# Kernel optimization log

Hardware: AMD Instinct MI355X
Metric: run time of the kernel (lower is better)

Reference implementation:

```python
import jax, jax.numpy as jnp
import numpy as np

B, N, DEG = 64, 512, 16        # graphs, nodes per graph, avg degree
C, HID = 10, 128               # input feat dim (== num_classes quirk), hidden
E = B * N * DEG                # total edges (fixed; pooling masks edges)


def _gcn(x, W, b, src, dst, emask, n):
    # PyG GCNConv: add self-loops, symmetric norm D^-1/2 (A+I) D^-1/2 (XW) + b
    h = x @ W
    deg = jax.ops.segment_sum(emask, dst, num_segments=n) + 1.0  # +1 self-loop
    dinv = jax.lax.rsqrt(deg)
    norm = dinv[src] * dinv[dst] * emask
    agg = jax.ops.segment_sum(h[src] * norm[:, None], dst, num_segments=n)
    return agg + h * (dinv * dinv)[:, None] + b  # self-loop term + bias


def _sag_pool(x, src, dst, emask, Wp, bp, n_per):
    # SAGPooling: score = tanh(GCN(x)); per-graph top-k (ratio=0.5); x' = x[perm]*score
    n = x.shape[0]
    score = jnp.tanh(_gcn(x, Wp, bp, src, dst, emask, n)[:, 0])
    k = n_per // 2
    vals, idx = jax.lax.top_k(score.reshape(B, n_per), k)  # [B,k]
    perm = (idx + (jnp.arange(B) * n_per)[:, None]).reshape(-1)
    xk = x[perm] * vals.reshape(-1)[:, None]
    # relabel edges; drop edges touching removed nodes via mask (fixed E)
    mapping = jnp.full((n,), -1, jnp.int32).at[perm].set(
        jnp.arange(B * k, dtype=jnp.int32))
    ns, nd = mapping[src], mapping[dst]
    nmask = emask * ((ns >= 0) & (nd >= 0)).astype(emask.dtype)
    return xk, jnp.maximum(ns, 0), jnp.maximum(nd, 0), nmask, k


def _readout(x, k):
    # global max pool || global mean pool (all kept nodes are real, no padding)
    xg = x.reshape(B, k, -1)
    return jnp.concatenate([xg.max(axis=1), xg.mean(axis=1)], axis=1)


def setup_inputs() -> dict:
    key = jax.random.key(0)
    ks = jax.random.split(key, 16)
    x = jax.random.normal(ks[0], (B * N, C), jnp.float32)
    off = jnp.repeat(jnp.arange(B, dtype=jnp.int32) * N, N * DEG)
    src = jax.random.randint(ks[1], (E,), 0, N, jnp.int32) + off
    dst = jax.random.randint(ks[2], (E,), 0, N, jnp.int32) + off
    p = lambda k, s: jax.random.normal(k, s, jnp.float32) * 0.05
    return {
        "x": x, "src": src, "dst": dst,
        "W1": p(ks[3], (C, HID)), "b1": jnp.zeros((HID,), jnp.float32),
        "W2": p(ks[4], (HID, HID)), "b2": jnp.zeros((HID,), jnp.float32),
        "W3": p(ks[5], (HID, HID)), "b3": jnp.zeros((HID,), jnp.float32),
        "Wp": p(ks[6], (HID, 1)), "bp": jnp.zeros((1,), jnp.float32),
        "L1W": p(ks[7], (2 * HID, HID)), "L1b": jnp.zeros((HID,), jnp.float32),
        "L2W": p(ks[8], (HID, HID // 2)), "L2b": jnp.zeros((HID // 2,), jnp.float32),
    }


def reference(x, src, dst, W1, b1, W2, b2, W3, b3, Wp, bp, L1W, L1b, L2W, L2b):
    emask = jnp.ones((E,), jnp.float32)
    h = jax.nn.relu(_gcn(x, W1, b1, src, dst, emask, B * N))
    h, src, dst, emask, k = _sag_pool(h, src, dst, emask, Wp, bp, N)
    x1 = _readout(h, k)
    h = jax.nn.relu(_gcn(h, W2, b2, src, dst, emask, B * k))
    h, src, dst, emask, k = _sag_pool(h, src, dst, emask, Wp, bp, k)
    x2 = _readout(h, k)
    h = jax.nn.relu(_gcn(h, W3, b3, src, dst, emask, B * k))
    h, src, dst, emask, k = _sag_pool(h, src, dst, emask, Wp, bp, k)
    x3 = _readout(h, k)
    z = x1 + x2 + x3
    z = jax.nn.relu(z @ L1W + L1b)
    # dropout inactive in eval mode
    z = jax.nn.relu(z @ L2W + L2b)
    return jax.nn.log_softmax(z, axis=1)
```

## Files before the change

kernel.cpp:

```cpp
#include <hip/hip_runtime.h>
#include <math.h>

#define BGR 64
#define N0 512
#define E_TOT (BGR*N0*16)
#define EPG 8192
#define EIT 16
#define HID 128
#define LOFF2 32768
#define LOFF3 49152

#define HSW(r,l) (((r)<<3) | (((l)+(r))&7))

__device__ __forceinline__ void bitonic_sort(float* sv, int* si, float v, int idx,
                                             int t, int nper, bool act){
  for (int kk = 2; kk <= nper; kk <<= 1){
    for (int jj = kk >> 1; jj > 0; jj >>= 1){
      if (jj >= 64){
        if (act){ sv[t] = v; si[t] = idx; }
        __syncthreads();
        if (act){
          int p = t ^ jj;
          float pv = sv[p]; int pi = si[p];
          bool amLower = (t & jj) == 0;
          bool dirDesc = (t & kk) == 0;
          bool betterMine = (v > pv) || (v == pv && idx < pi);
          if ((amLower == dirDesc) != betterMine){ v = pv; idx = pi; }
        }
        __syncthreads();
      } else if (act){
        float pv = __shfl_xor(v, jj);
        int   pi = __shfl_xor(idx, jj);
        bool amLower = (t & jj) == 0;
        bool dirDesc = (t & kk) == 0;
        bool betterMine = (v > pv) || (v == pv && idx < pi);
        if ((amLower == dirDesc) != betterMine){ v = pv; idx = pi; }
      }
    }
  }
  if (act){ sv[t] = v; si[t] = idx; }
  __syncthreads();
}

__device__ __forceinline__ void relabel_pre(
    int2* __restrict__ edges, int2* __restrict__ csr, const int* si,
    int* map_, int* sb, int* cur, float* dl, int* wsum,
    int* __restrict__ rowptr, int* __restrict__ cnt, float* __restrict__ dinv,
    const int2* epre,
    int t, int nper, int k, int gbase, int gbnew, int ebase, int loff){
  if (t < nper) map_[t] = -1;
  if (t < k) sb[t] = 0;
  __syncthreads();
  if (t < k) map_[si[t]] = t;
  __syncthreads();
  int2 ebuf[8];
  #pragma unroll
  for (int it = 0; it < 8; it++){
    int2 e = epre[it];
    int2 ne = make_int2(-1, 0);
    if (e.x >= 0){
      int ns = map_[e.x - gbase], nd = map_[e.y - gbase];
      if (ns >= 0 && nd >= 0){
        ne = make_int2(gbnew + ns, gbnew + nd);
        atomicAdd(&sb[nd], 1);
      }
    }
    ebuf[it] = ne;
    edges[ebase + it*1024 + t] = ne;
  }
  __syncthreads();
  int vdeg = (t < k) ? sb[t] : 0;
  int lane = t & 63, wid = t >> 6;
  int x = vdeg;
  #pragma unroll
  for (int off = 1; off < 64; off <<= 1){
    int y = __shfl_up(x, off);
    if (lane >= off) x += y;
  }
  if (t < k && lane == 63) wsum[wid] = x;
  __syncthreads();
  if (t < k){
    int prefix = 0;
    #pragma unroll
    for (int wj = 0; wj < 4; wj++) prefix += (wj < wid) ? wsum[wj] : 0;
    int excl = x + prefix - vdeg;
    rowptr[loff + gbnew + t] = ebase + excl;
    cnt[loff + gbnew + t] = vdeg;
    cur[t] = excl;
    float dv = rsqrtf((float)vdeg + 1.f);
    dl[t] = dv;
    dinv[loff + gbnew + t] = dv;
  }
  __syncthreads();
  #pragma unroll
  for (int it = 0; it < 8; it++){
    int2 e = ebuf[it];
    if (e.x >= 0){
      int sl = e.x - gbnew, dc = e.y - gbnew;
      int pos = atomicAdd(&cur[dc], 1);
      csr[ebase + pos] = make_int2(e.x, __float_as_int(dl[sl]*dl[dc]));
    }
  }
  __syncthreads();
}

__global__ __launch_bounds__(512) void k_topo0(
    const int* __restrict__ s0, const int* __restrict__ d0,
    int2* __restrict__ edges, int* __restrict__ cnt, int* __restrict__ rowptr,
    float* __restrict__ dinv, int2* __restrict__ csr){
  __shared__ int   deg[512];
  __shared__ int   cur[512];
  __shared__ float dl[512];
  __shared__ int   wsum[8];
  int g = (blockIdx.x & 7)*8 + (blockIdx.x >> 3);
  int t = threadIdx.x;
  int gbase = g*N0, ebase = g*EPG;
  deg[t] = 0;
  __syncthreads();
  int2 ebuf[EIT];
  #pragma unroll
  for (int it = 0; it < EIT; it++){
    int i = ebase + it*512 + t;
    int2 e = make_int2(s0[i], d0[i]);
    ebuf[it] = e;
    edges[i] = e;
    atomicAdd(&deg[e.y - gbase], 1);
  }
  __syncthreads();
  int vdeg = deg[t];
  int lane = t & 63, wid = t >> 6;
  int x = vdeg;
  #pragma unroll
  for (int off = 1; off < 64; off <<= 1){
    int y = __shfl_up(x, off);
    if (lane >= off) x += y;
  }
  if (lane == 63) wsum[wid] = x;
  __syncthreads();
  int prefix = 0;
  #pragma unroll
  for (int wj = 0; wj < 8; wj++) prefix += (wj < wid) ? wsum[wj] : 0;
  int excl = x + prefix - vdeg;
  rowptr[gbase + t] = ebase + excl;
  cnt[gbase + t] = vdeg;
  cur[t] = excl;
  float dv = rsqrtf((float)vdeg + 1.f);
  dl[t] = dv;
  dinv[gbase + t] = dv;
  __syncthreads();
  #pragma unroll
  for (int it = 0; it < EIT; it++){
    int2 e = ebuf[it];
    int sl = e.x - gbase, dc = e.y - gbase;
    int pos = atomicAdd(&cur[dc], 1);
    csr[ebase + pos] = make_int2(e.x, __float_as_int(dl[sl]*dl[dc]));
  }
}

__global__ __launch_bounds__(512) void k_l1_fused(
    const float* __restrict__ x, const float* __restrict__ W1,
    const int2* __restrict__ csr, const int* __restrict__ rowptr,
    const int* __restrict__ cnt, const float* __restrict__ dinv,
    const float* __restrict__ b1, const float* __restrict__ Wp,
    float4* __restrict__ gout4, float* __restrict__ hp_part){
  extern __shared__ float hl[];
  int b = blockIdx.x;
  int xcd = b & 7, idx = b >> 3;
  int graph = xcd*8 + (idx >> 3);
  int sub = idx & 7;
  int qf = sub >> 1, half = sub & 1;
  int t = threadIdx.x;
  int gbase = graph*N0;
  int fp = t & 31;
  int f = qf*32 + fp;
  float wcol[10];
  #pragma unroll
  for (int k = 0; k < 10; k++) wcol[k] = W1[k*HID + f];
  for (int n = t >> 5; n < N0; n += 16){
    const float* xr = x + (gbase + n)*10;
    float acc = 0.f;
    #pragma unroll
    for (int k = 0; k < 10; k++) acc += xr[k]*wcol[k];
    hl[n*32 + ((((fp>>2)+n)&7)<<2) + (fp&3)] = acc;
  }
  __syncthreads();
  const float4* hl4 = (const float4*)hl;
  int l = t & 7, grp = t >> 3;
  float4 bb = ((const float4*)b1)[qf*8 + l];
  float4 wp = ((const float4*)Wp)[qf*8 + l];
  int n0 = half*256;
  for (int nl = n0 + grp; nl < n0 + 256; nl += 64){
    int node = gbase + nl;
    int start = rowptr[node], c = cnt[node];
    float4 acc = make_float4(0.f,0.f,0.f,0.f);
    int j = 0;
    for (; j + 4 <= c; j += 4){
      int2 e0 = csr[start+j],   e1 = csr[start+j+1];
      int2 e2 = csr[start+j+2], e3 = csr[start+j+3];
      float4 h0 = hl4[HSW(e0.x - gbase, l)];
      float4 h1 = hl4[HSW(e1.x - gbase, l)];
      float4 h2 = hl4[HSW(e2.x - gbase, l)];
      float4 h3 = hl4[HSW(e3.x - gbase, l)];
      float w0 = __int_as_float(e0.y), w1 = __int_as_float(e1.y);
      float w2 = __int_as_float(e2.y), w3 = __int_as_float(e3.y);
      acc.x += w0*h0.x + w1*h1.x + w2*h2.x + w3*h3.x;
      acc.y += w0*h0.y + w1*h1.y + w2*h2.y + w3*h3.y;
      acc.z += w0*h0.z + w1*h1.z + w2*h2.z + w3*h3.z;
      acc.w += w0*h0.w + w1*h1.w + w2*h2.w + w3*h3.w;
    }
    for (; j < c; j++){
      int2 e = csr[start + j];
      float wgt = __int_as_float(e.y);
      float4 hv = hl4[HSW(e.x - gbase, l)];
      acc.x += wgt*hv.x; acc.y += wgt*hv.y; acc.z += wgt*hv.z; acc.w += wgt*hv.w;
    }
    float di = dinv[node], dd = di*di;
    float4 hs = hl4[HSW(nl, l)];
    float4 v;
    v.x = fmaxf(acc.x + hs.x*dd + bb.x, 0.f);
    v.y = fmaxf(acc.y + hs.y*dd + bb.y, 0.f);
    v.z = fmaxf(acc.z + hs.z*dd + bb.z, 0.f);
    v.w = fmaxf(acc.w + hs.w*dd + bb.w, 0.f);
    gout4[node*32 + qf*8 + l] = v;
    float contrib = v.x*wp.x + v.y*wp.y + v.z*wp.z + v.w*wp.w;
    #pragma unroll
    for (int off = 4; off; off >>= 1) contrib += __shfl_down(contrib, off, 8);
    if (l == 0) hp_part[qf*32768 + node] = contrib;
  }
}

__global__ __launch_bounds__(1024) void k_mega1(
    const float4* __restrict__ gout4, const float* __restrict__ hppt,
    int2* __restrict__ csr, int* __restrict__ rowptr, int* __restrict__ cnt,
    float* __restrict__ dinv, const float* __restrict__ bp,
    int2* __restrict__ edges, int* __restrict__ sig, float* __restrict__ svg,
    float* __restrict__ z){
  __shared__ float sv[512];
  __shared__ int   si[512];
  __shared__ float hpl[512];
  __shared__ union UA {
    float spart[1024];
    struct { float4 pmx[16][32]; float4 psm[16][32]; } ro;
    struct { int map_[512]; int sb[512]; int cur[256]; } rl;
  } u;
  __shared__ float dl[256];
  __shared__ int   wsum[4];
  int g = (blockIdx.x & 7)*8 + (blockIdx.x >> 3);
  int t = threadIdx.x;
  int gbase = g*N0, ebase = g*EPG, gb2 = g*256;
  float bp0 = bp[0];
  int2 epre[8];
  #pragma unroll
  for (int it = 0; it < 8; it++) epre[it] = edges[ebase + it*1024 + t];
  if (t < 512){
    int node = gbase + t;
    hpl[t] = hppt[node] + hppt[32768+node] + hppt[65536+node] + hppt[98304+node];
  }
  __syncthreads();
  {
    int n = t & 511, p = t >> 9;
    int start = rowptr[gbase + n], c = cnt[gbase + n];
    int lo = (c*p) >> 1, hi = (c*(p+1)) >> 1;
    float a = 0.f;
    for (int j = lo; j < hi; j++){
      int2 e = csr[start + j];
      a += __int_as_float(e.y)*hpl[e.x - gbase];
    }
    u.spart[t] = a;
  }
  __syncthreads();
  float v = 0.f; int idx = t;
  if (t < 512){
    float a = u.spart[t] + u.spart[t + 512];
    float di = dinv[gbase + t];
    v = tanhf(a + hpl[t]*di*di + bp0);
  }
  __syncthreads();
  bitonic_sort(sv, si, v, idx, t, 512, t < 512);
  if (t < 256){ sig[g*512 + t] = si[t]; svg[g*512 + t] = sv[t]; }
  int l = t & 31, j0 = t >> 5;
  if (t < 512){
    float4 mx = make_float4(-INFINITY,-INFINITY,-INFINITY,-INFINITY);
    float4 sm = make_float4(0.f,0.f,0.f,0.f);
    for (int j = j0; j < 256; j += 16){
      float val = sv[j]; int row = si[j];
      float4 hv = gout4[(gbase + row)*32 + l];
      float4 o = make_float4(hv.x*val, hv.y*val, hv.z*val, hv.w*val);
      mx.x = fmaxf(mx.x, o.x); mx.y = fmaxf(mx.y, o.y);
      mx.z = fmaxf(mx.z, o.z); mx.w = fmaxf(mx.w, o.w);
      sm.x += o.x; sm.y += o.y; sm.z += o.z; sm.w += o.w;
    }
    u.ro.pmx[j0][l] = mx; u.ro.psm[j0][l] = sm;
  }
  __syncthreads();
  if (t < 32){
    float4 M = u.ro.pmx[0][t], S = u.ro.psm[0][t];
    #pragma unroll
    for (int q = 1; q < 16; q++){
      float4 m2 = u.ro.pmx[q][t], s2 = u.ro.psm[q][t];
      M.x = fmaxf(M.x, m2.x); M.y = fmaxf(M.y, m2.y);
      M.z = fmaxf(M.z, m2.z); M.w = fmaxf(M.w, m2.w);
      S.x += s2.x; S.y += s2.y; S.z += s2.z; S.w += s2.w;
    }
    float ki = 1.f/256.f;
    float* zp = z + g*256;
    zp[t*4+0] = M.x; zp[t*4+1] = M.y; zp[t*4+2] = M.z; zp[t*4+3] = M.w;
    zp[128+t*4+0] = S.x*ki; zp[128+t*4+1] = S.y*ki;
    zp[128+t*4+2] = S.z*ki; zp[128+t*4+3] = S.w*ki;
  }
  __syncthreads();
  relabel_pre(edges, csr, si, u.rl.map_, u.rl.sb, u.rl.cur, dl, wsum,
              rowptr, cnt, dinv, epre, t, 512, 256, gbase, gb2, ebase, LOFF2);
}

__global__ __launch_bounds__(512) void k_lvl2(
    const float4* __restrict__ gout4,
    const int* __restrict__ sig, const float* __restrict__ svg,
    const float* __restrict__ W2, const float* __restrict__ b2,
    const float* __restrict__ Wp,
    const int2* __restrict__ csr, const int* __restrict__ rowptr,
    const int* __restrict__ cnt, const float* __restrict__ dinv,
    float4* __restrict__ g2out4, float* __restrict__ hp2){
  __shared__ float hL[256*HID];
  int b = blockIdx.x;
  int jb = b & 63, sub = b >> 6;
  int g = (jb & 7)*8 + (jb >> 3);
  int t = threadIdx.x;
  int gbase = g*N0, gb2 = g*256;
  {
    int foct = t & 15, rg = t >> 4;
    int f0 = foct*8, rbase = rg*8;
    int ri[8]; float rv[8];
    #pragma unroll
    for (int q = 0; q < 8; q++){
      ri[q] = sig[g*512 + rbase + q];
      rv[q] = svg[g*512 + rbase + q];
    }
    float4 accA[8], accB[8];
    #pragma unroll
    for (int q = 0; q < 8; q++){
      accA[q] = make_float4(0.f,0.f,0.f,0.f);
      accB[q] = make_float4(0.f,0.f,0.f,0.f);
    }
    for (int i = 0; i < HID; i += 4){
      float4 wa[4], wb[4];
      #pragma unroll
      for (int ii = 0; ii < 4; ii++){
        wa[ii] = *(const float4*)(W2 + (i+ii)*HID + f0);
        wb[ii] = *(const float4*)(W2 + (i+ii)*HID + f0 + 4);
      }
      #pragma unroll
      for (int q = 0; q < 8; q++){
        float4 xv = gout4[(gbase + ri[q])*32 + (i>>2)];
        float vx = xv.x*rv[q], vy = xv.y*rv[q], vz = xv.z*rv[q], vw = xv.w*rv[q];
        accA[q].x += vx*wa[0].x + vy*wa[1].x + vz*wa[2].x + vw*wa[3].x;
        accA[q].y += vx*wa[0].y + vy*wa[1].y + vz*wa[2].y + vw*wa[3].y;
        accA[q].z += vx*wa[0].z + vy*wa[1].z + vz*wa[2].z + vw*wa[3].z;
        accA[q].w += vx*wa[0].w + vy*wa[1].w + vz*wa[2].w + vw*wa[3].w;
        accB[q].x += vx*wb[0].x + vy*wb[1].x + vz*wb[2].x + vw*wb[3].x;
        accB[q].y += vx*wb[0].y + vy*wb[1].y + vz*wb[2].y + vw*wb[3].y;
        accB[q].z += vx*wb[0].z + vy*wb[1].z + vz*wb[2].z + vw*wb[3].z;
        accB[q].w += vx*wb[0].w + vy*wb[1].w + vz*wb[2].w + vw*wb[3].w;
      }
    }
    #pragma unroll
    for (int q = 0; q < 8; q++){
      *(float4*)(hL + (rbase+q)*HID + f0) = accA[q];
      *(float4*)(hL + (rbase+q)*HID + f0 + 4) = accB[q];
    }
  }
  __syncthreads();
  const float4* hL4 = (const float4*)hL;
  int l = t & 31, grpn = t >> 5;
  float4 bb = ((const float4*)b2)[l];
  float4 wp = ((const float4*)Wp)[l];
  for (int it = 0; it < 4; it++){
    int n = sub*64 + it*16 + grpn;
    int node = gb2 + n;
    int start = rowptr[LOFF2 + node], c = cnt[LOFF2 + node];
    float4 acc = make_float4(0.f,0.f,0.f,0.f);
    int j = 0;
    for (; j + 4 <= c; j += 4){
      int2 e0 = csr[start+j],   e1 = csr[start+j+1];
      int2 e2 = csr[start+j+2], e3 = csr[start+j+3];
      float4 h0 = hL4[(e0.x - gb2)*32 + l];
      float4 h1 = hL4[(e1.x - gb2)*32 + l];
      float4 h2 = hL4[(e2.x - gb2)*32 + l];
      float4 h3 = hL4[(e3.x - gb2)*32 + l];
      float w0 = __int_as_float(e0.y), w1 = __int_as_float(e1.y);
      float w2 = __int_as_float(e2.y), w3 = __int_as_float(e3.y);
      acc.x += w0*h0.x + w1*h1.x + w2*h2.x + w3*h3.x;
      acc.y += w0*h0.y + w1*h1.y + w2*h2.y + w3*h3.y;
      acc.z += w0*h0.z + w1*h1.z + w2*h2.z + w3*h3.z;
      acc.w += w0*h0.w + w1*h1.w + w2*h2.w + w3*h3.w;
    }
    for (; j < c; j++){
      int2 e = csr[start + j];
      float wgt = __int_as_float(e.y);
      float4 hv = hL4[(e.x - gb2)*32 + l];
      acc.x += wgt*hv.x; acc.y += wgt*hv.y; acc.z += wgt*hv.z; acc.w += wgt*hv.w;
    }
    float di = dinv[LOFF2 + node], dd = di*di;
    float4 hs = hL4[n*32 + l];
    float4 v;
    v.x = fmaxf(acc.x + hs.x*dd + bb.x, 0.f);
    v.y = fmaxf(acc.y + hs.y*dd + bb.y, 0.f);
    v.z = fmaxf(acc.z + hs.z*dd + bb.z, 0.f);
    v.w = fmaxf(acc.w + hs.w*dd + bb.w, 0.f);
    g2out4[node*32 + l] = v;
    float contrib = v.x*wp.x + v.y*wp.y + v.z*wp.z + v.w*wp.w;
    #pragma unroll
    for (int off = 16; off; off >>= 1) contrib += __shfl_down(contrib, off, 32);
    if (l == 0) hp2[node] = contrib;
  }
}

__global__ __launch_bounds__(1024) void k_mega2(
    const float4* __restrict__ g2out4, const float* __restrict__ hp2,
    int2* __restrict__ csr, int* __restrict__ rowptr, int* __restrict__ cnt,
    float* __restrict__ dinv, const float* __restrict__ bp,
    int2* __restrict__ edges, int* __restrict__ sig, float* __restrict__ svg,
    float* __restrict__ z){
  __shared__ float sv[256];
  __shared__ int   si[256];
  __shared__ float hpl[256];
  __shared__ union UB {
    float spart[1024];
    struct { float4 pmx[16][32]; float4 psm[16][32]; } ro;
    struct { int map_[256]; int sb[128]; int cur[128]; } rl;
  } u;
  __shared__ float dl[128];
  __shared__ int   wsum[4];
  int g = (blockIdx.x & 7)*8 + (blockIdx.x >> 3);
  int t = threadIdx.x;
  int gb2 = g*256, gb3 = g*128, ebase = g*EPG;
  float bp0 = bp[0];
  int2 epre[8];
  #pragma unroll
  for (int it = 0; it < 8; it++) epre[it] = edges[ebase + it*1024 + t];
  if (t < 256) hpl[t] = hp2[gb2 + t];
  __syncthreads();
  {
    int n = t & 255, p = t >> 8;
    int start = rowptr[LOFF2 + gb2 + n], c = cnt[LOFF2 + gb2 + n];
    int lo = (c*p) >> 2, hi = (c*(p+1)) >> 2;
    float a = 0.f;
    for (int j = lo; j < hi; j++){
      int2 e = csr[start + j];
      a += __int_as_float(e.y)*hpl[e.x - gb2];
    }
    u.spart[t] = a;
  }
  __syncthreads();
  float v = 0.f; int idx = t;
  if (t < 256){
    float a = u.spart[t] + u.spart[t+256] + u.spart[t+512] + u.spart[t+768];
    float di = dinv[LOFF2 + gb2 + t];
    v = tanhf(a + hpl[t]*di*di + bp0);
  }
  __syncthreads();
  bitonic_sort(sv, si, v, idx, t, 256, t < 256);
  if (t < 128){ sig[g*512 + t] = si[t]; svg[g*512 + t] = sv[t]; }
  int l = t & 31, j0 = t >> 5;
  if (t < 512){
    float4 mx = make_float4(-INFINITY,-INFINITY,-INFINITY,-INFINITY);
    float4 sm = make_float4(0.f,0.f,0.f,0.f);
    for (int j = j0; j < 128; j += 16){
      float val = sv[j]; int row = si[j];
      float4 hv = g2out4[(gb2 + row)*32 + l];
      float4 o = make_float4(hv.x*val, hv.y*val, hv.z*val, hv.w*val);
      mx.x = fmaxf(mx.x, o.x); mx.y = fmaxf(mx.y, o.y);
      mx.z = fmaxf(mx.z, o.z); mx.w = fmaxf(mx.w, o.w);
      sm.x += o.x; sm.y += o.y; sm.z += o.z; sm.w += o.w;
    }
    u.ro.pmx[j0][l] = mx; u.ro.psm[j0][l] = sm;
  }
  __syncthreads();
  if (t < 32){
    float4 M = u.ro.pmx[0][t], S = u.ro.psm[0][t];
    #pragma unroll
    for (int q = 1; q < 16; q++){
      float4 m2 = u.ro.pmx[q][t], s2 = u.ro.psm[q][t];
      M.x = fmaxf(M.x, m2.x); M.y = fmaxf(M.y, m2.y);
      M.z = fmaxf(M.z, m2.z); M.w = fmaxf(M.w, m2.w);
      S.x += s2.x; S.y += s2.y; S.z += s2.z; S.w += s2.w;
    }
    float ki = 1.f/128.f;
    float* zp = z + g*256;
    zp[t*4+0] += M.x; zp[t*4+1] += M.y; zp[t*4+2] += M.z; zp[t*4+3] += M.w;
    zp[128+t*4+0] += S.x*ki; zp[128+t*4+1] += S.y*ki;
    zp[128+t*4+2] += S.z*ki; zp[128+t*4+3] += S.w*ki;
  }
  __syncthreads();
  relabel_pre(edges, csr, si, u.rl.map_, u.rl.sb, u.rl.cur, dl, wsum,
              rowptr, cnt, dinv, epre, t, 256, 128, gb2, gb3, ebase, LOFF3);
}

__global__ __launch_bounds__(512) void k_lvl3(
    const float4* __restrict__ g2out4,
    const int* __restrict__ sig, const float* __restrict__ svg,
    const float* __restrict__ W3, const float* __restrict__ b3,
    const float* __restrict__ Wp,
    const int2* __restrict__ csr, const int* __restrict__ rowptr,
    const int* __restrict__ cnt, const float* __restrict__ dinv,
    float4* __restrict__ g3out4, float* __restrict__ hp3){
  __shared__ float hL[128*HID];
  int b = blockIdx.x;
  int jb = b & 63, sub = b >> 6;
  int g = (jb & 7)*8 + (jb >> 3);
  int t = threadIdx.x;
  int gb2 = g*256, gb3 = g*128;
  {
    int foct = t & 15, rg = t >> 4;
    int f0 = foct*8, rbase = rg*4;
    int ri[4]; float rv[4];
    #pragma unroll
    for (int q = 0; q < 4; q++){
      ri[q] = sig[g*512 + rbase + q];
      rv[q] = svg[g*512 + rbase + q];
    }
    float4 accA[4], accB[4];
    #pragma unroll
    for (int q = 0; q < 4; q++){
      accA[q] = make_float4(0.f,0.f,0.f,0.f);
      accB[q] = make_float4(0.f,0.f,0.f,0.f);
    }
    for (int i = 0; i < HID; i += 4){
      float4 wa[4], wb[4];
      #pragma unroll
      for (int ii = 0; ii < 4; ii++){
        wa[ii] = *(const float4*)(W3 + (i+ii)*HID + f0);
        wb[ii] = *(const float4*)(W3 + (i+ii)*HID + f0 + 4);
      }
      #pragma unroll
      for (int q = 0; q < 4; q++){
        float4 xv = g2out4[(gb2 + ri[q])*32 + (i>>2)];
        float vx = xv.x*rv[q], vy = xv.y*rv[q], vz = xv.z*rv[q], vw = xv.w*rv[q];
        accA[q].x += vx*wa[0].x + vy*wa[1].x + vz*wa[2].x + vw*wa[3].x;
        accA[q].y += vx*wa[0].y + vy*wa[1].y + vz*wa[2].y + vw*wa[3].y;
        accA[q].z += vx*wa[0].z + vy*wa[1].z + vz*wa[2].z + vw*wa[3].z;
        accA[q].w += vx*wa[0].w + vy*wa[1].w + vz*wa[2].w + vw*wa[3].w;
        accB[q].x += vx*wb[0].x + vy*wb[1].x + vz*wb[2].x + vw*wb[3].x;
        accB[q].y += vx*wb[0].y + vy*wb[1].y + vz*wb[2].y + vw*wb[3].y;
        accB[q].z += vx*wb[0].z + vy*wb[1].z + vz*wb[2].z + vw*wb[3].z;
        accB[q].w += vx*wb[0].w + vy*wb[1].w + vz*wb[2].w + vw*wb[3].w;
      }
    }
    #pragma unroll
    for (int q = 0; q < 4; q++){
      *(float4*)(hL + (rbase+q)*HID + f0) = accA[q];
      *(float4*)(hL + (rbase+q)*HID + f0 + 4) = accB[q];
    }
  }
  __syncthreads();
  const float4* hL4 = (const float4*)hL;
  int l = t & 31, grpn = t >> 5;
  float4 bb = ((const float4*)b3)[l];
  float4 wp = ((const float4*)Wp)[l];
  for (int it = 0; it < 2; it++){
    int n = sub*32 + it*16 + grpn;
    int node = gb3 + n;
    int start = rowptr[LOFF3 + node], c = cnt[LOFF3 + node];
    float4 acc = make_float4(0.f,0.f,0.f,0.f);
    int j = 0;
    for (; j + 4 <= c; j += 4){
      int2 e0 = csr[start+j],   e1 = csr[start+j+1];
      int2 e2 = csr[start+j+2], e3 = csr[start+j+3];
      float4 h0 = hL4[(e0.x - gb3)*32 + l];
      float4 h1 = hL4[(e1.x - gb3)*32 + l];
      float4 h2 = hL4[(e2.x - gb3)*32 + l];
      float4 h3 = hL4[(e3.x - gb3)*32 + l];
      float w0 = __int_as_float(e0.y), w1 = __int_as_float(e1.y);
      float w2 = __int_as_float(e2.y), w3 = __int_as_float(e3.y);
      acc.x += w0*h0.x + w1*h1.x + w2*h2.x + w3*h3.x;
      acc.y += w0*h0.y + w1*h1.y + w2*h2.y + w3*h3.y;
      acc.z += w0*h0.z + w1*h1.z + w2*h2.z + w3*h3.z;
      acc.w += w0*h0.w + w1*h1.w + w2*h2.w + w3*h3.w;
    }
    for (; j < c; j++){
      int2 e = csr[start + j];
      float wgt = __int_as_float(e.y);
      float4 hv = hL4[(e.x - gb3)*32 + l];
      acc.x += wgt*hv.x; acc.y += wgt*hv.y; acc.z += wgt*hv.z; acc.w += wgt*hv.w;
    }
    float di = dinv[LOFF3 + node], dd = di*di;
    float4 hs = hL4[n*32 + l];
    float4 v;
    v.x = fmaxf(acc.x + hs.x*dd + bb.x, 0.f);
    v.y = fmaxf(acc.y + hs.y*dd + bb.y, 0.f);
    v.z = fmaxf(acc.z + hs.z*dd + bb.z, 0.f);
    v.w = fmaxf(acc.w + hs.w*dd + bb.w, 0.f);
    g3out4[node*32 + l] = v;
    float contrib = v.x*wp.x + v.y*wp.y + v.z*wp.z + v.w*wp.w;
    #pragma unroll
    for (int off = 16; off; off >>= 1) contrib += __shfl_down(contrib, off, 32);
    if (l == 0) hp3[node] = contrib;
  }
}

__global__ __launch_bounds__(1024) void k_mega3(
    const float4* __restrict__ g3out4, const float* __restrict__ hp3,
    const int2* __restrict__ csr, const int* __restrict__ rowptr,
    const int* __restrict__ cnt, const float* __restrict__ dinv,
    const float* __restrict__ bp, float* __restrict__ z,
    const float* __restrict__ L1W, const float* __restrict__ L1b,
    const float* __restrict__ L2W, const float* __restrict__ L2b,
    float* __restrict__ out){
  __shared__ float sv[128];
  __shared__ int   si[128];
  __shared__ float hpl[128];
  __shared__ union UC {
    float spart[1024];
    struct { float4 pmx[16][32]; float4 psm[16][32]; } ro;
  } u;
  __shared__ float zr[256];
  __shared__ float h1l[128];
  __shared__ float h2l[64];
  __shared__ float red[2];
  int g = (blockIdx.x & 7)*8 + (blockIdx.x >> 3);
  int t = threadIdx.x;
  int gb3 = g*128;
  float bp0 = bp[0];
  if (t < 128) hpl[t] = hp3[gb3 + t];
  __syncthreads();
  {
    int n = t & 127, p = t >> 7;
    int start = rowptr[LOFF3 + gb3 + n], c = cnt[LOFF3 + gb3 + n];
    int lo = (c*p) >> 3, hi = (c*(p+1)) >> 3;
    float a = 0.f;
    for (int j = lo; j < hi; j++){
      int2 e = csr[start + j];
      a += __int_as_float(e.y)*hpl[e.x - gb3];
    }
    u.spart[t] = a;
  }
  __syncthreads();
  float v = 0.f; int idx = t;
  if (t < 128){
    float a = 0.f;
    #pragma unroll
    for (int pp = 0; pp < 8; pp++) a += u.spart[t + pp*128];
    float di = dinv[LOFF3 + gb3 + t];
    v = tanhf(a + hpl[t]*di*di + bp0);
  }
  __syncthreads();
  bitonic_sort(sv, si, v, idx, t, 128, t < 128);
  int l = t & 31, j0 = t >> 5;
  if (t < 512){
    float4 mx = make_float4(-INFINITY,-INFINITY,-INFINITY,-INFINITY);
    float4 sm = make_float4(0.f,0.f,0.f,0.f);
    for (int j = j0; j < 64; j += 16){
      float val = sv[j]; int row = si[j];
      float4 hv = g3out4[(gb3 + row)*32 + l];
      float4 o = make_float4(hv.x*val, hv.y*val, hv.z*val, hv.w*val);
      mx.x = fmaxf(mx.x, o.x); mx.y = fmaxf(mx.y, o.y);
      mx.z = fmaxf(mx.z, o.z); mx.w = fmaxf(mx.w, o.w);
      sm.x += o.x; sm.y += o.y; sm.z += o.z; sm.w += o.w;
    }
    u.ro.pmx[j0][l] = mx; u.ro.psm[j0][l] = sm;
  }
  __syncthreads();
  if (t < 32){
    float4 M = u.ro.pmx[0][t], S = u.ro.psm[0][t];
    #pragma unroll
    for (int q = 1; q < 16; q++){
      float4 m2 = u.ro.pmx[q][t], s2 = u.ro.psm[q][t];
      M.x = fmaxf(M.x, m2.x); M.y = fmaxf(M.y, m2.y);
      M.z = fmaxf(M.z, m2.z); M.w = fmaxf(M.w, m2.w);
      S.x += s2.x; S.y += s2.y; S.z += s2.z; S.w += s2.w;
    }
    float ki = 1.f/64.f;
    float* zp = z + g*256;
    zr[t*4+0] = zp[t*4+0] + M.x; zr[t*4+1] = zp[t*4+1] + M.y;
    zr[t*4+2] = zp[t*4+2] + M.z; zr[t*4+3] = zp[t*4+3] + M.w;
    zr[128+t*4+0] = zp[128+t*4+0] + S.x*ki;
    zr[128+t*4+1] = zp[128+t*4+1] + S.y*ki;
    zr[128+t*4+2] = zp[128+t*4+2] + S.z*ki;
    zr[128+t*4+3] = zp[128+t*4+3] + S.w*ki;
  }
  __syncthreads();
  if (t < 128){
    float a = L1b[t];
    for (int i = 0; i < 256; i++) a += zr[i]*L1W[i*128 + t];
    h1l[t] = fmaxf(a, 0.f);
  }
  __syncthreads();
  if (t < 64){
    float a = L2b[t];
    for (int i = 0; i < 128; i++) a += h1l[i]*L2W[i*64 + t];
    h2l[t] = fmaxf(a, 0.f);
  }
  __syncthreads();
  if (t == 0){
    float mxv = -INFINITY;
    for (int i = 0; i < 64; i++) mxv = fmaxf(mxv, h2l[i]);
    float s = 0.f;
    for (int i = 0; i < 64; i++) s += expf(h2l[i] - mxv);
    red[0] = mxv; red[1] = logf(s);
  }
  __syncthreads();
  if (t < 64) out[g*64 + t] = h2l[t] - red[0] - red[1];
}

extern "C" void kernel_launch(void* const* d_in, const int* in_sizes, int n_in,
                              void* d_out, int out_size, void* d_ws, size_t ws_size,
                              hipStream_t stream){
  (void)in_sizes; (void)n_in; (void)out_size; (void)ws_size;
  const float* x0  = (const float*)d_in[0];
  const int*   s0  = (const int*)  d_in[1];
  const int*   d0  = (const int*)  d_in[2];
  const float* W1  = (const float*)d_in[3];  const float* b1 = (const float*)d_in[4];
  const float* W2  = (const float*)d_in[5];  const float* b2 = (const float*)d_in[6];
  const float* W3  = (const float*)d_in[7];  const float* b3 = (const float*)d_in[8];
  const float* Wp  = (const float*)d_in[9];  const float* bp = (const float*)d_in[10];
  const float* L1W = (const float*)d_in[11]; const float* L1b = (const float*)d_in[12];
  const float* L2W = (const float*)d_in[13]; const float* L2b = (const float*)d_in[14];
  float* out = (float*)d_out;

  float* w = (float*)d_ws;
  float* gout1 = w; w += 32768*HID;
  float* gout2 = w; w += 16384*HID;
  float* gout3 = w; w += 8192*HID;
  float* dinvv = w; w += 65536;
  float* hppt  = w; w += 4*32768;
  float* hp2   = w; w += 16384;
  float* hp3   = w; w += 8192;
  float* z     = w; w += BGR*256;
  float* svg   = w; w += 32768;
  int* sig     = (int*)w; w += 32768;
  int* cnt     = (int*)w; w += 65536;
  int* rowptr  = (int*)w; w += 65536;
  int2* edges  = (int2*)w; w += 2*E_TOT;
  int2* csr    = (int2*)w; w += 2*E_TOT;

  k_topo0<<<BGR, 512, 0, stream>>>(s0, d0, edges, cnt, rowptr, dinvv, csr);
  k_l1_fused<<<512, 512, 65536, stream>>>(x0, W1, csr, rowptr, cnt, dinvv,
                                          b1, Wp, (float4*)gout1, hppt);
  k_mega1<<<BGR, 1024, 0, stream>>>((const float4*)gout1, hppt, csr, rowptr,
                                    cnt, dinvv, bp, edges, sig, svg, z);
  k_lvl2<<<4*BGR, 512, 0, stream>>>((const float4*)gout1, sig, svg, W2, b2, Wp,
                                    csr, rowptr, cnt, dinvv,
                                    (float4*)gout2, hp2);
  k_mega2<<<BGR, 1024, 0, stream>>>((const float4*)gout2, hp2, csr, rowptr,
                                    cnt, dinvv, bp, edges, sig, svg, z);
  k_lvl3<<<4*BGR, 512, 0, stream>>>((const float4*)gout2, sig, svg, W3, b3, Wp,
                                    csr, rowptr, cnt, dinvv,
                                    (float4*)gout3, hp3);
  k_mega3<<<BGR, 1024, 0, stream>>>((const float4*)gout3, hp3, csr, rowptr,
                                    cnt, dinvv, bp, z,
                                    L1W, L1b, L2W, L2b, out);
}
```

Before: 257.8 us.

## Split level-2/3 GCN blocks by feature slice instead of node slice

```diff
diff --git a/kernel.cpp b/kernel.cpp
--- a/kernel.cpp
+++ b/kernel.cpp
@@ -320,62 +320,51 @@
     const float* __restrict__ Wp,
     const int2* __restrict__ csr, const int* __restrict__ rowptr,
     const int* __restrict__ cnt, const float* __restrict__ dinv,
-    float4* __restrict__ g2out4, float* __restrict__ hp2){
-  __shared__ float hL[256*HID];
+    float4* __restrict__ g2out4, float* __restrict__ hp2p){
+  __shared__ float hL[256*32];
   int b = blockIdx.x;
-  int jb = b & 63, sub = b >> 6;
+  int jb = b & 63, s = b >> 6;
   int g = (jb & 7)*8 + (jb >> 3);
   int t = threadIdx.x;
   int gbase = g*N0, gb2 = g*256;
+  float4* hL4 = (float4*)hL;
   {
-    int foct = t & 15, rg = t >> 4;
-    int f0 = foct*8, rbase = rg*8;
-    int ri[8]; float rv[8];
-    #pragma unroll
-    for (int q = 0; q < 8; q++){
+    int f4 = t & 7, rg = t >> 3;
+    int rbase = rg*4;
+    const float* Wb = W2 + s*32 + f4*4;
+    int ri[4]; float rv[4];
+    #pragma unroll
+    for (int q = 0; q < 4; q++){
       ri[q] = sig[g*512 + rbase + q];
       rv[q] = svg[g*512 + rbase + q];
     }
-    float4 accA[8], accB[8];
-    #pragma unroll
-    for (int q = 0; q < 8; q++){
-      accA[q] = make_float4(0.f,0.f,0.f,0.f);
-      accB[q] = make_float4(0.f,0.f,0.f,0.f);
-    }
+    float4 acc[4];
+    #pragma unroll
+    for (int q = 0; q < 4; q++) acc[q] = make_float4(0.f,0.f,0.f,0.f);
     for (int i = 0; i < HID; i += 4){
-      float4 wa[4], wb[4];
+      float4 w0 = *(const float4*)(Wb + (i+0)*HID);
+      float4 w1 = *(const float4*)(Wb + (i+1)*HID);
+      float4 w2 = *(const float4*)(Wb + (i+2)*HID);
+      float4 w3 = *(const float4*)(Wb + (i+3)*HID);
       #pragma unroll
-      for (int ii = 0; ii < 4; ii++){
-        wa[ii] = *(const float4*)(W2 + (i+ii)*HID + f0);
-        wb[ii] = *(const float4*)(W2 + (i+ii)*HID + f0 + 4);
-      }
-      #pragma unroll
-      for (int q = 0; q < 8; q++){
+      for (int q = 0; q < 4; q++){
         float4 xv = gout4[(gbase + ri[q])*32 + (i>>2)];
         float vx = xv.x*rv[q], vy = xv.y*rv[q], vz = xv.z*rv[q], vw = xv.w*rv[q];
-        accA[q].x += vx*wa[0].x + vy*wa[1].x + vz*wa[2].x + vw*wa[3].x;
-        accA[q].y += vx*wa[0].y + vy*wa[1].y + vz*wa[2].y + vw*wa[3].y;
-        accA[q].z += vx*wa[0].z + vy*wa[1].z + vz*wa[2].z + vw*wa[3].z;
-        accA[q].w += vx*wa[0].w + vy*wa[1].w + vz*wa[2].w + vw*wa[3].w;
-        accB[q].x += vx*wb[0].x + vy*wb[1].x + vz*wb[2].x + vw*wb[3].x;
-        accB[q].y += vx*wb[0].y + vy*wb[1].y + vz*wb[2].y + vw*wb[3].y;
-        accB[q].z += vx*wb[0].z + vy*wb[1].z + vz*wb[2].z + vw*wb[3].z;
-        accB[q].w += vx*wb[0].w + vy*wb[1].w + vz*wb[2].w + vw*wb[3].w;
+        acc[q].x += vx*w0.x + vy*w1.x + vz*w2.x + vw*w3.x;
+        acc[q].y += vx*w0.y + vy*w1.y + vz*w2.y + vw*w3.y;
+        acc[q].z += vx*w0.z + vy*w1.z + vz*w2.z + vw*w3.z;
+        acc[q].w += vx*w0.w + vy*w1.w + vz*w2.w + vw*w3.w;
       }
     }
     #pragma unroll
-    for (int q = 0; q < 8; q++){
-      *(float4*)(hL + (rbase+q)*HID + f0) = accA[q];
-      *(float4*)(hL + (rbase+q)*HID + f0 + 4) = accB[q];
-    }
-  }
-  __syncthreads();
-  const float4* hL4 = (const float4*)hL;
-  int l = t & 31, grpn = t >> 5;
-  float4 bb = ((const float4*)b2)[l];
-  float4 wp = ((const float4*)Wp)[l];
+    for (int q = 0; q < 4; q++) hL4[HSW(rbase+q, f4)] = acc[q];
+  }
+  __syncthreads();
+  int l = t & 7, grpn = t >> 3;
+  float4 bb = ((const float4*)b2)[s*8 + l];
+  float4 wp = ((const float4*)Wp)[s*8 + l];
   for (int it = 0; it < 4; it++){
-    int n = sub*64 + it*16 + grpn;
+    int n = it*64 + grpn;
     int node = gb2 + n;
     int start = rowptr[LOFF2 + node], c = cnt[LOFF2 + node];
     float4 acc = make_float4(0.f,0.f,0.f,0.f);
@@ -383,10 +372,10 @@
     for (; j + 4 <= c; j += 4){
       int2 e0 = csr[start+j],   e1 = csr[start+j+1];
       int2 e2 = csr[start+j+2], e3 = csr[start+j+3];
-      float4 h0 = hL4[(e0.x - gb2)*32 + l];
-      float4 h1 = hL4[(e1.x - gb2)*32 + l];
-      float4 h2 = hL4[(e2.x - gb2)*32 + l];
-      float4 h3 = hL4[(e3.x - gb2)*32 + l];
+      float4 h0 = hL4[HSW(e0.x - gb2, l)];
+      float4 h1 = hL4[HSW(e1.x - gb2, l)];
+      float4 h2 = hL4[HSW(e2.x - gb2, l)];
+      float4 h3 = hL4[HSW(e3.x - gb2, l)];
       float w0 = __int_as_float(e0.y), w1 = __int_as_float(e1.y);
       float w2 = __int_as_float(e2.y), w3 = __int_as_float(e3.y);
       acc.x += w0*h0.x + w1*h1.x + w2*h2.x + w3*h3.x;
@@ -397,26 +386,26 @@
     for (; j < c; j++){
       int2 e = csr[start + j];
       float wgt = __int_as_float(e.y);
-      float4 hv = hL4[(e.x - gb2)*32 + l];
+      float4 hv = hL4[HSW(e.x - gb2, l)];
       acc.x += wgt*hv.x; acc.y += wgt*hv.y; acc.z += wgt*hv.z; acc.w += wgt*hv.w;
     }
     float di = dinv[LOFF2 + node], dd = di*di;
-    float4 hs = hL4[n*32 + l];
+    float4 hs = hL4[HSW(n, l)];
     float4 v;
     v.x = fmaxf(acc.x + hs.x*dd + bb.x, 0.f);
     v.y = fmaxf(acc.y + hs.y*dd + bb.y, 0.f);
     v.z = fmaxf(acc.z + hs.z*dd + bb.z, 0.f);
     v.w = fmaxf(acc.w + hs.w*dd + bb.w, 0.f);
-    g2out4[node*32 + l] = v;
+    g2out4[node*32 + s*8 + l] = v;
     float contrib = v.x*wp.x + v.y*wp.y + v.z*wp.z + v.w*wp.w;
     #pragma unroll
-    for (int off = 16; off; off >>= 1) contrib += __shfl_down(contrib, off, 32);
-    if (l == 0) hp2[node] = contrib;
+    for (int off = 4; off; off >>= 1) contrib += __shfl_down(contrib, off, 8);
+    if (l == 0) hp2p[s*16384 + node] = contrib;
   }
 }
 
 __global__ __launch_bounds__(1024) void k_mega2(
-    const float4* __restrict__ g2out4, const float* __restrict__ hp2,
+    const float4* __restrict__ g2out4, const float* __restrict__ hp2p,
     int2* __restrict__ csr, int* __restrict__ rowptr, int* __restrict__ cnt,
     float* __restrict__ dinv, const float* __restrict__ bp,
     int2* __restrict__ edges, int* __restrict__ sig, float* __restrict__ svg,
@@ -438,7 +427,10 @@
   int2 epre[8];
   #pragma unroll
   for (int it = 0; it < 8; it++) epre[it] = edges[ebase + it*1024 + t];
-  if (t < 256) hpl[t] = hp2[gb2 + t];
+  if (t < 256){
+    int node = gb2 + t;
+    hpl[t] = hp2p[node] + hp2p[16384+node] + hp2p[32768+node] + hp2p[49152+node];
+  }
   __syncthreads();
   {
     int n = t & 255, p = t >> 8;
@@ -503,62 +495,51 @@
     const float* __restrict__ Wp,
     const int2* __restrict__ csr, const int* __restrict__ rowptr,
     const int* __restrict__ cnt, const float* __restrict__ dinv,
-    float4* __restrict__ g3out4, float* __restrict__ hp3){
-  __shared__ float hL[128*HID];
+    float4* __restrict__ g3out4, float* __restrict__ hp3p){
+  __shared__ float hL[128*32];
   int b = blockIdx.x;
-  int jb = b & 63, sub = b >> 6;
+  int jb = b & 63, s = b >> 6;
   int g = (jb & 7)*8 + (jb >> 3);
   int t = threadIdx.x;
   int gb2 = g*256, gb3 = g*128;
+  float4* hL4 = (float4*)hL;
   {
-    int foct = t & 15, rg = t >> 4;
-    int f0 = foct*8, rbase = rg*4;
-    int ri[4]; float rv[4];
-    #pragma unroll
-    for (int q = 0; q < 4; q++){
+    int f4 = t & 7, rg = t >> 3;
+    int rbase = rg*2;
+    const float* Wb = W3 + s*32 + f4*4;
+    int ri[2]; float rv[2];
+    #pragma unroll
+    for (int q = 0; q < 2; q++){
       ri[q] = sig[g*512 + rbase + q];
       rv[q] = svg[g*512 + rbase + q];
     }
-    float4 accA[4], accB[4];
-    #pragma unroll
-    for (int q = 0; q < 4; q++){
-      accA[q] = make_float4(0.f,0.f,0.f,0.f);
-      accB[q] = make_float4(0.f,0.f,0.f,0.f);
-    }
+    float4 acc[2];
+    #pragma unroll
+    for (int q = 0; q < 2; q++) acc[q] = make_float4(0.f,0.f,0.f,0.f);
     for (int i = 0; i < HID; i += 4){
-      float4 wa[4], wb[4];
+      float4 w0 = *(const float4*)(Wb + (i+0)*HID);
+      float4 w1 = *(const float4*)(Wb + (i+1)*HID);
+      float4 w2 = *(const float4*)(Wb + (i+2)*HID);
+      float4 w3 = *(const float4*)(Wb + (i+3)*HID);
       #pragma unroll
-      for (int ii = 0; ii < 4; ii++){
-        wa[ii] = *(const float4*)(W3 + (i+ii)*HID + f0);
-        wb[ii] = *(const float4*)(W3 + (i+ii)*HID + f0 + 4);
-      }
-      #pragma unroll
-      for (int q = 0; q < 4; q++){
+      for (int q = 0; q < 2; q++){
         float4 xv = g2out4[(gb2 + ri[q])*32 + (i>>2)];
         float vx = xv.x*rv[q], vy = xv.y*rv[q], vz = xv.z*rv[q], vw = xv.w*rv[q];
-        accA[q].x += vx*wa[0].x + vy*wa[1].x + vz*wa[2].x + vw*wa[3].x;
-        accA[q].y += vx*wa[0].y + vy*wa[1].y + vz*wa[2].y + vw*wa[3].y;
-        accA[q].z += vx*wa[0].z + vy*wa[1].z + vz*wa[2].z + vw*wa[3].z;
-        accA[q].w += vx*wa[0].w + vy*wa[1].w + vz*wa[2].w + vw*wa[3].w;
-        accB[q].x += vx*wb[0].x + vy*wb[1].x + vz*wb[2].x + vw*wb[3].x;
-        accB[q].y += vx*wb[0].y + vy*wb[1].y + vz*wb[2].y + vw*wb[3].y;
-        accB[q].z += vx*wb[0].z + vy*wb[1].z + vz*wb[2].z + vw*wb[3].z;
-        accB[q].w += vx*wb[0].w + vy*wb[1].w + vz*wb[2].w + vw*wb[3].w;
+        acc[q].x += vx*w0.x + vy*w1.x + vz*w2.x + vw*w3.x;
+        acc[q].y += vx*w0.y + vy*w1.y + vz*w2.y + vw*w3.y;
+        acc[q].z += vx*w0.z + vy*w1.z + vz*w2.z + vw*w3.z;
+        acc[q].w += vx*w0.w + vy*w1.w + vz*w2.w + vw*w3.w;
       }
     }
     #pragma unroll
-    for (int q = 0; q < 4; q++){
-      *(float4*)(hL + (rbase+q)*HID + f0) = accA[q];
-      *(float4*)(hL + (rbase+q)*HID + f0 + 4) = accB[q];
-    }
-  }
-  __syncthreads();
-  const float4* hL4 = (const float4*)hL;
-  int l = t & 31, grpn = t >> 5;
-  float4 bb = ((const float4*)b3)[l];
-  float4 wp = ((const float4*)Wp)[l];
+    for (int q = 0; q < 2; q++) hL4[HSW(rbase+q, f4)] = acc[q];
+  }
+  __syncthreads();
+  int l = t & 7, grpn = t >> 3;
+  float4 bb = ((const float4*)b3)[s*8 + l];
+  float4 wp = ((const float4*)Wp)[s*8 + l];
   for (int it = 0; it < 2; it++){
-    int n = sub*32 + it*16 + grpn;
+    int n = it*64 + grpn;
     int node = gb3 + n;
     int start = rowptr[LOFF3 + node], c = cnt[LOFF3 + node];
     float4 acc = make_float4(0.f,0.f,0.f,0.f);
@@ -566,10 +547,10 @@
     for (; j + 4 <= c; j += 4){
       int2 e0 = csr[start+j],   e1 = csr[start+j+1];
       int2 e2 = csr[start+j+2], e3 = csr[start+j+3];
-      float4 h0 = hL4[(e0.x - gb3)*32 + l];
-      float4 h1 = hL4[(e1.x - gb3)*32 + l];
-      float4 h2 = hL4[(e2.x - gb3)*32 + l];
-      float4 h3 = hL4[(e3.x - gb3)*32 + l];
+      float4 h0 = hL4[HSW(e0.x - gb3, l)];
+      float4 h1 = hL4[HSW(e1.x - gb3, l)];
+      float4 h2 = hL4[HSW(e2.x - gb3, l)];
+      float4 h3 = hL4[HSW(e3.x - gb3, l)];
       float w0 = __int_as_float(e0.y), w1 = __int_as_float(e1.y);
       float w2 = __int_as_float(e2.y), w3 = __int_as_float(e3.y);
       acc.x += w0*h0.x + w1*h1.x + w2*h2.x + w3*h3.x;
@@ -580,26 +561,26 @@
     for (; j < c; j++){
       int2 e = csr[start + j];
       float wgt = __int_as_float(e.y);
-      float4 hv = hL4[(e.x - gb3)*32 + l];
+      float4 hv = hL4[HSW(e.x - gb3, l)];
       acc.x += wgt*hv.x; acc.y += wgt*hv.y; acc.z += wgt*hv.z; acc.w += wgt*hv.w;
     }
     float di = dinv[LOFF3 + node], dd = di*di;
-    float4 hs = hL4[n*32 + l];
+    float4 hs = hL4[HSW(n, l)];
     float4 v;
     v.x = fmaxf(acc.x + hs.x*dd + bb.x, 0.f);
     v.y = fmaxf(acc.y + hs.y*dd + bb.y, 0.f);
     v.z = fmaxf(acc.z + hs.z*dd + bb.z, 0.f);
     v.w = fmaxf(acc.w + hs.w*dd + bb.w, 0.f);
-    g3out4[node*32 + l] = v;
+    g3out4[node*32 + s*8 + l] = v;
     float contrib = v.x*wp.x + v.y*wp.y + v.z*wp.z + v.w*wp.w;
     #pragma unroll
-    for (int off = 16; off; off >>= 1) contrib += __shfl_down(contrib, off, 32);
-    if (l == 0) hp3[node] = contrib;
+    for (int off = 4; off; off >>= 1) contrib += __shfl_down(contrib, off, 8);
+    if (l == 0) hp3p[s*8192 + node] = contrib;
   }
 }
 
 __global__ __launch_bounds__(1024) void k_mega3(
-    const float4* __restrict__ g3out4, const float* __restrict__ hp3,
+    const float4* __restrict__ g3out4, const float* __restrict__ hp3p,
     const int2* __restrict__ csr, const int* __restrict__ rowptr,
     const int* __restrict__ cnt, const float* __restrict__ dinv,
     const float* __restrict__ bp, float* __restrict__ z,
@@ -621,7 +602,10 @@
   int t = threadIdx.x;
   int gb3 = g*128;
   float bp0 = bp[0];
-  if (t < 128) hpl[t] = hp3[gb3 + t];
+  if (t < 128){
+    int node = gb3 + t;
+    hpl[t] = hp3p[node] + hp3p[8192+node] + hp3p[16384+node] + hp3p[24576+node];
+  }
   __syncthreads();
   {
     int n = t & 127, p = t >> 7;
@@ -723,8 +707,8 @@
   float* gout3 = w; w += 8192*HID;
   float* dinvv = w; w += 65536;
   float* hppt  = w; w += 4*32768;
-  float* hp2   = w; w += 16384;
-  float* hp3   = w; w += 8192;
+  float* hp2p  = w; w += 4*16384;
+  float* hp3p  = w; w += 4*8192;
   float* z     = w; w += BGR*256;
   float* svg   = w; w += 32768;
   int* sig     = (int*)w; w += 32768;
@@ -740,13 +724,13 @@
                                     cnt, dinvv, bp, edges, sig, svg, z);
   k_lvl2<<<4*BGR, 512, 0, stream>>>((const float4*)gout1, sig, svg, W2, b2, Wp,
                                     csr, rowptr, cnt, dinvv,
-                                    (float4*)gout2, hp2);
-  k_mega2<<<BGR, 1024, 0, stream>>>((const float4*)gout2, hp2, csr, rowptr,
+                                    (float4*)gout2, hp2p);
+  k_mega2<<<BGR, 1024, 0, stream>>>((const float4*)gout2, hp2p, csr, rowptr,
                                     cnt, dinvv, bp, edges, sig, svg, z);
   k_lvl3<<<4*BGR, 512, 0, stream>>>((const float4*)gout2, sig, svg, W3, b3, Wp,
                                     csr, rowptr, cnt, dinvv,
-                                    (float4*)gout3, hp3);
-  k_mega3<<<BGR, 1024, 0, stream>>>((const float4*)gout3, hp3, csr, rowptr,
+                                    (float4*)gout3, hp3p);
+  k_mega3<<<BGR, 1024, 0, stream>>>((const float4*)gout3, hp3p, csr, rowptr,
                                     cnt, dinvv, bp, z,
                                     L1W, L1b, L2W, L2b, out);
 }
```

Measured after the change: 233.6 us. 1.1x faster.
